# Performance work log

Hardware: AMD Instinct MI355X
Metric: run time of the kernel (lower is better)

Reference implementation:

```python
import jax, jax.numpy as jnp
import numpy as np

N, D, NH, NC, B, NL = 400, 256, 4, 2, 64, 2
HD = D // NH


def _ln(x, g, b, eps=1e-5):
    mu = x.mean(-1, keepdims=True)
    var = ((x - mu) ** 2).mean(-1, keepdims=True)
    return (x - mu) * jax.lax.rsqrt(var + eps) * g + b


def _mha(q, kv, wqkv, bqkv, wo, bo):
    # torch nn.MultiheadAttention (batch_first), eval mode
    wq, wk, wv = jnp.split(wqkv, 3, axis=0)
    bq, bk, bv = jnp.split(bqkv, 3, axis=0)
    Bsz, Sq, _ = q.shape
    Sk = kv.shape[1]
    qh = (q @ wq.T + bq).reshape(Bsz, Sq, NH, HD).transpose(0, 2, 1, 3)
    kh = (kv @ wk.T + bk).reshape(Bsz, Sk, NH, HD).transpose(0, 2, 1, 3)
    vh = (kv @ wv.T + bv).reshape(Bsz, Sk, NH, HD).transpose(0, 2, 1, 3)
    scores = jnp.einsum('bhqd,bhkd->bhqk', qh, kh) / jnp.sqrt(jnp.float32(HD))
    attn = jax.nn.softmax(scores, axis=-1)
    o = jnp.einsum('bhqk,bhkd->bhqd', attn, vh)
    o = o.transpose(0, 2, 1, 3).reshape(Bsz, Sq, D)
    return o @ wo.T + bo


def setup_inputs() -> dict:
    key = jax.random.key(0)
    ks = iter(jax.random.split(key, 64))
    w = lambda *s: (jax.random.normal(next(ks), s, dtype=jnp.float32) * 0.02)
    inp = {
        'fc_matrix': jax.random.uniform(next(ks), (B, N, N), dtype=jnp.float32),
        'sc_matrix': jax.random.uniform(next(ks), (B, N, N), dtype=jnp.float32),
        'proj_w': w(D, N), 'proj_b': jnp.zeros((D,), jnp.float32),
        'enc_qkv_w': w(NL, 3 * D, D), 'enc_qkv_b': jnp.zeros((NL, 3 * D), jnp.float32),
        'enc_out_w': w(NL, D, D), 'enc_out_b': jnp.zeros((NL, D), jnp.float32),
        'enc_lin1_w': w(NL, 4 * D, D), 'enc_lin1_b': jnp.zeros((NL, 4 * D), jnp.float32),
        'enc_lin2_w': w(NL, D, 4 * D), 'enc_lin2_b': jnp.zeros((NL, D), jnp.float32),
        'enc_n1_g': jnp.ones((NL, D), jnp.float32), 'enc_n1_b': jnp.zeros((NL, D), jnp.float32),
        'enc_n2_g': jnp.ones((NL, D), jnp.float32), 'enc_n2_b': jnp.zeros((NL, D), jnp.float32),
        'gcn_w1': w(D, N), 'gcn_b1': jnp.zeros((D,), jnp.float32),
        'gcn_w2': w(D, D), 'gcn_b2': jnp.zeros((D,), jnp.float32),
        'ca1_qkv_w': w(3 * D, D), 'ca1_qkv_b': jnp.zeros((3 * D,), jnp.float32),
        'ca1_out_w': w(D, D), 'ca1_out_b': jnp.zeros((D,), jnp.float32),
        'ca1_n_g': jnp.ones((D,), jnp.float32), 'ca1_n_b': jnp.zeros((D,), jnp.float32),
        'ca2_qkv_w': w(3 * D, D), 'ca2_qkv_b': jnp.zeros((3 * D,), jnp.float32),
        'ca2_out_w': w(D, D), 'ca2_out_b': jnp.zeros((D,), jnp.float32),
        'ca2_n_g': jnp.ones((D,), jnp.float32), 'ca2_n_b': jnp.zeros((D,), jnp.float32),
        'cls_w1': w(128, N * D), 'cls_b1': jnp.zeros((128,), jnp.float32),
        'cls_w2': w(NC, 128), 'cls_b2': jnp.zeros((NC,), jnp.float32),
    }
    return inp


def reference(fc_matrix, sc_matrix, proj_w, proj_b,
              enc_qkv_w, enc_qkv_b, enc_out_w, enc_out_b,
              enc_lin1_w, enc_lin1_b, enc_lin2_w, enc_lin2_b,
              enc_n1_g, enc_n1_b, enc_n2_g, enc_n2_b,
              gcn_w1, gcn_b1, gcn_w2, gcn_b2,
              ca1_qkv_w, ca1_qkv_b, ca1_out_w, ca1_out_b, ca1_n_g, ca1_n_b,
              ca2_qkv_w, ca2_qkv_b, ca2_out_w, ca2_out_b, ca2_n_g, ca2_n_b,
              cls_w1, cls_b1, cls_w2, cls_b2):
    # ---- FC branch: input proj + 2 post-norm transformer encoder layers ----
    h = fc_matrix @ proj_w.T + proj_b  # [B,N,D]
    for l in range(NL):
        a = _mha(h, h, enc_qkv_w[l], enc_qkv_b[l], enc_out_w[l], enc_out_b[l])
        h = _ln(h + a, enc_n1_g[l], enc_n1_b[l])
        ff = jax.nn.relu(h @ enc_lin1_w[l].T + enc_lin1_b[l]) @ enc_lin2_w[l].T + enc_lin2_b[l]
        h = _ln(h + ff, enc_n2_g[l], enc_n2_b[l])
    Z_F = h

    # ---- SC branch: dense-equivalent of per-sample nonzero()+GCNConv ----
    # all entries of sc are nonzero -> edge set == dense adjacency (self-loops present,
    # so add_remaining_self_loops is a no-op). deg = in-degree (column sums of weights).
    deg = sc_matrix.sum(axis=-2)  # [B,N]
    dinv = jnp.where(deg > 0, jax.lax.rsqrt(deg), 0.0)
    An = dinv[:, :, None] * sc_matrix * dinv[:, None, :]  # An[b,i,j] = dinv_i * w_ij * dinv_j
    h1 = jnp.einsum('bij,bid->bjd', An, sc_matrix @ gcn_w1.T) + gcn_b1  # aggregate src->dst
    h1 = jax.nn.relu(h1)
    Z_S = jnp.einsum('bij,bid->bjd', An, h1 @ gcn_w2.T) + gcn_b2  # [B,N,D]

    # ---- Cross attention (eval: dropout = identity) ----
    Z_F_cross = _ln(Z_F + _mha(Z_F, Z_S, ca1_qkv_w, ca1_qkv_b, ca1_out_w, ca1_out_b), ca1_n_g, ca1_n_b)
    Z_S_cross = _ln(Z_S + _mha(Z_S, Z_F, ca2_qkv_w, ca2_qkv_b, ca2_out_w, ca2_out_b), ca2_n_g, ca2_n_b)

    Z_joint = (Z_F_cross + Z_S_cross) * 0.5
    flat = Z_joint.reshape(Z_joint.shape[0], -1)  # [B, N*D]
    logits = jax.nn.relu(flat @ cls_w1.T + cls_b1) @ cls_w2.T + cls_b2
    return logits
```

## Files before the change

kernel.cpp:

```cpp
#include <hip/hip_runtime.h>
#include <math.h>

#define NB   64
#define NN   400
#define DD   256
#define NHH  4
#define HDD  64
#define MR   25600

typedef __attribute__((ext_vector_type(8))) short bf16x8;
typedef __attribute__((ext_vector_type(4))) float f32x4;

__device__ __forceinline__ short f2bf(float x) {
    union { float f; unsigned u; } v; v.f = x;
    return (short)((v.u + 0x7FFFu + ((v.u >> 16) & 1u)) >> 16);
}
__device__ __forceinline__ float bf2f(short s) {
    union { unsigned u; float f; } v; v.u = ((unsigned)(unsigned short)s) << 16;
    return v.f;
}
__device__ __forceinline__ void gl_lds16(const void* g, void* l) {
    __builtin_amdgcn_global_load_lds(
        (const __attribute__((address_space(1))) unsigned*)g,
        (__attribute__((address_space(3))) unsigned*)l, 16, 0, 0);
}
__device__ __forceinline__ void wait_vmcnt(int n) {
    switch (n) {
    case 0: asm volatile("s_waitcnt vmcnt(0)" ::: "memory"); break;
    case 1: asm volatile("s_waitcnt vmcnt(1)" ::: "memory"); break;
    case 2: asm volatile("s_waitcnt vmcnt(2)" ::: "memory"); break;
    case 3: asm volatile("s_waitcnt vmcnt(3)" ::: "memory"); break;
    case 4: asm volatile("s_waitcnt vmcnt(4)" ::: "memory"); break;
    default: asm volatile("s_waitcnt vmcnt(5)" ::: "memory"); break;
    }
}
__device__ __forceinline__ void barrier_raw() {
    __builtin_amdgcn_sched_barrier(0);
    __builtin_amdgcn_s_barrier();
    __builtin_amdgcn_sched_barrier(0);
}


__global__ __launch_bounds__(256) void gemm_p8(
    const short* __restrict__ A, int arows, long long sA,
    const short* __restrict__ B, int brows, long long sB,
    const float* __restrict__ bias,
    short* __restrict__ C, int crows, int crz, long long sCe,
    int M, int N, int Npad, int K, int relu)
{
    __shared__ short lds[24576];
    const int tid = threadIdx.x;
    const int z = blockIdx.z;
    const int m0 = blockIdx.x * 128, n0 = blockIdx.y * 128;
    const short* Ab = A + (size_t)z * sA;
    const short* Bb = B + (size_t)z * sB;

    const int w = tid >> 6, lane = tid & 63;
    const int quad = lane >> 4, l15 = lane & 15;
    const int wm = w & 1, wn = w >> 1;

    f32x4 acc[4][4] = {};

    const int KT = K >> 5;

    auto STAGE = [&](int buf, int kt) {
        const int gp0 = kt << 2;
        short* Al = lds + buf * 8192;
        short* Bl = Al + 4096;
#pragma unroll
        for (int i = 0; i < 4; ++i) {
            int c = i * 4 + w;
            int p = (c >> 1) & 3, hh = c & 1;
            if (c < 8)
                gl_lds16(Ab + ((size_t)(gp0 + p) * arows + m0 + hh * 64 + lane) * 8,
                         &Al[(p * 128 + hh * 64) * 8]);
            else
                gl_lds16(Bb + ((size_t)(gp0 + p) * brows + n0 + hh * 64 + lane) * 8,
                         &Bl[(p * 128 + hh * 64) * 8]);
        }
    };

    STAGE(0, 0);
    STAGE(1, 1);
    for (int kt = 0; kt < KT; ++kt) {
        wait_vmcnt(kt + 1 < KT ? 4 : 0);
        barrier_raw();
        if (kt + 2 < KT) STAGE((kt + 2) % 3, kt + 2);
        const short* Al = lds + (kt % 3) * 8192;
        const short* Bl = Al + 4096;
        bf16x8 af[4], bfr[4];
#pragma unroll
        for (int mi = 0; mi < 4; ++mi)
            af[mi] = *reinterpret_cast<const bf16x8*>(
                &Al[(quad * 128 + wm * 64 + mi * 16 + l15) * 8]);
#pragma unroll
        for (int ni = 0; ni < 4; ++ni)
            bfr[ni] = *reinterpret_cast<const bf16x8*>(
                &Bl[(quad * 128 + wn * 64 + ni * 16 + l15) * 8]);
#pragma unroll
        for (int mi = 0; mi < 4; ++mi)
#pragma unroll
            for (int ni = 0; ni < 4; ++ni)
                acc[mi][ni] = __builtin_amdgcn_mfma_f32_16x16x32_bf16(af[mi], bfr[ni], acc[mi][ni], 0, 0, 0);
    }
    __syncthreads();

#pragma unroll
    for (int mi = 0; mi < 4; ++mi) {
#pragma unroll
        for (int r = 0; r < 4; ++r) {
            int row = wm * 64 + mi * 16 + quad * 4 + r;
#pragma unroll
            for (int ni = 0; ni < 4; ++ni) {
                int col = wn * 64 + ni * 16 + l15;
                int gcol = n0 + col;
                float v = 0.0f;
                if (gcol < N) {
                    v = acc[mi][ni][r];
                    if (bias) v += bias[gcol];
                    if (relu) v = fmaxf(v, 0.0f);
                }
                lds[row * 136 + col] = f2bf(v);
            }
        }
    }
    __syncthreads();
    short* Cbz = C + (size_t)z * sCe;
    const long long zr = (long long)z * crz;
#pragma unroll
    for (int t = 0; t < 8; ++t) {
        int c = t * 256 + tid;
        int row = c & 127, p16 = c >> 7;
        int grow = m0 + row;
        int gcol0 = n0 + p16 * 8;
        if (grow < M && gcol0 < Npad) {
            bf16x8 v = *reinterpret_cast<const bf16x8*>(&lds[row * 136 + p16 * 8]);
            *reinterpret_cast<bf16x8*>(
                &Cbz[((size_t)(gcol0 >> 3) * crows + zr + grow) * 8]) = v;
        }
    }
}

__global__ __launch_bounds__(256) void gemm_ln(
    const short* __restrict__ A,
    const short* __restrict__ B, int brows,
    const float* __restrict__ bias,
    const short* __restrict__ resid,
    const float* __restrict__ g, const float* __restrict__ bb,
    short* __restrict__ out, int K)
{
    __shared__ short lds[30720];
    __shared__ float gs[256], bs[256], bi_s[256];
    __shared__ float red[2][4][64];
    const int tid = threadIdx.x;
    const int m0 = blockIdx.x * 64;
    const int w = tid >> 6, lane = tid & 63;
    const int quad = lane >> 4, l15 = lane & 15;
    gs[tid] = g[tid]; bs[tid] = bb[tid]; bi_s[tid] = bias[tid];

    f32x4 acc[16] = {};
    const int KT = K >> 5;

    auto STAGE = [&](int buf, int kt) {
        const int gp0 = kt << 2;
        short* Al = lds + buf * 10240;
        short* Bl = Al + 2048;
#pragma unroll
        for (int i = 0; i < 5; ++i) {
            int c = i * 4 + w;
            if (c < 4) {
                gl_lds16(A + ((size_t)(gp0 + c) * MR + m0 + lane) * 8, &Al[(c * 64) * 8]);
            } else {
                int cb = c - 4, p = cb >> 2, cq = cb & 3;
                gl_lds16(B + ((size_t)(gp0 + p) * brows + cq * 64 + lane) * 8,
                         &Bl[(p * 256 + cq * 64) * 8]);
            }
        }
    };

    STAGE(0, 0);
    STAGE(1, 1);
    for (int kt = 0; kt < KT; ++kt) {
        wait_vmcnt(kt + 1 < KT ? 5 : 0);
        barrier_raw();
        if (kt + 2 < KT) STAGE((kt + 2) % 3, kt + 2);
        const short* Al = lds + (kt % 3) * 10240;
        const short* Bl = Al + 2048;
        bf16x8 af = *reinterpret_cast<const bf16x8*>(
            &Al[(quad * 64 + w * 16 + l15) * 8]);
#pragma unroll
        for (int ni = 0; ni < 16; ++ni) {
            bf16x8 bfr = *reinterpret_cast<const bf16x8*>(
                &Bl[(quad * 256 + ni * 16 + l15) * 8]);
            acc[ni] = __builtin_amdgcn_mfma_f32_16x16x32_bf16(af, bfr, acc[ni], 0, 0, 0);
        }
    }
    __syncthreads();

    short* rowt = lds;
#pragma unroll
    for (int ni = 0; ni < 16; ++ni) {
        int col = ni * 16 + l15;
        int part = col >> 6, idx = col & 63;
#pragma unroll
        for (int r = 0; r < 4; ++r) {
            int row = w * 16 + quad * 4 + r;
            rowt[row * 264 + part * 66 + idx] = f2bf(acc[ni][r] + bi_s[col]);
        }
    }
    __syncthreads();

    const int row = tid >> 2, part = tid & 3;
    const int grow = m0 + row;
    float vv[8][8];
    float sum = 0.0f, sq = 0.0f;
#pragma unroll
    for (int i = 0; i < 8; ++i) {
        int plane = part * 8 + i;
        bf16x8 rv = *reinterpret_cast<const bf16x8*>(resid + ((size_t)plane * MR + grow) * 8);
        bf16x8 tv = *reinterpret_cast<const bf16x8*>(&rowt[row * 264 + part * 66 + i * 8]);
#pragma unroll
        for (int e = 0; e < 8; ++e) {
            float v = bf2f(tv[e]) + bf2f(rv[e]);
            vv[i][e] = v; sum += v; sq += v * v;
        }
    }
    red[0][part][row] = sum; red[1][part][row] = sq;
    __syncthreads();
    sum = red[0][0][row] + red[0][1][row] + red[0][2][row] + red[0][3][row];
    sq  = red[1][0][row] + red[1][1][row] + red[1][2][row] + red[1][3][row];
    float mu = sum * (1.0f / 256.0f);
    float var = sq * (1.0f / 256.0f) - mu * mu;
    float rstd = 1.0f / sqrtf(fmaxf(var, 0.0f) + 1e-5f);
#pragma unroll
    for (int i = 0; i < 8; ++i) {
        int plane = part * 8 + i;
        bf16x8 o;
#pragma unroll
        for (int e = 0; e < 8; ++e)
            o[e] = f2bf((vv[i][e] - mu) * rstd * gs[plane * 8 + e] + bs[plane * 8 + e]);
        *reinterpret_cast<bf16x8*>(out + ((size_t)plane * MR + grow) * 8) = o;
    }
}

__global__ __launch_bounds__(256) void vtrans(
    const short* __restrict__ qkv, short* __restrict__ vT)
{
    __shared__ short tile[64][66];
    const int id = blockIdx.x;
    const int xcd = id & 7, rem = id >> 3;
    const int bh_hi = rem / 7, c = rem - bh_hi * 7;
    const int bh_i = bh_hi * 8 + xcd;
    const int h = bh_i & 3, b = bh_i >> 2;
    const int tid = threadIdx.x;
    const size_t bh = (size_t)bh_i;
    for (int t = tid; t < 512; t += 256) {
        int pp = t >> 6, l = t & 63;
        int j = c * 64 + l;
        bf16x8 v;
        if (j < NN)
            v = *reinterpret_cast<const bf16x8*>(
                qkv + (((size_t)(64 + 8 * h + pp)) * MR + (size_t)b * NN + j) * 8);
        else { for (int e = 0; e < 8; ++e) v[e] = 0; }
#pragma unroll
        for (int e = 0; e < 8; ++e) tile[l][pp * 8 + e] = v[e];
    }
    __syncthreads();
    for (int t = tid; t < 512; t += 256) {
        int kq = t >> 6, d = t & 63;
        int kp = c * 8 + kq;
        bf16x8 o;
#pragma unroll
        for (int e = 0; e < 8; ++e) o[e] = tile[kq * 8 + e][d];
        *reinterpret_cast<bf16x8*>(vT + ((bh * 56 + kp) * 64 + d) * 8) = o;
    }
}

__global__ __launch_bounds__(256) void attn_p8(
    const short* __restrict__ qkv, const short* __restrict__ vT,
    short* __restrict__ Out)
{
    __shared__ short KP[8 * 448 * 8];
    __shared__ short QV[5][2048];
    const int id = blockIdx.x;
    const int xcd = id & 7, rem = id >> 3;
    const int bh_hi = rem / 7, qt = rem - bh_hi * 7;
    const int bh_i = bh_hi * 8 + xcd;
    const int h = bh_i & 3, b = bh_i >> 2;
    const int tid = threadIdx.x;
    const int w = tid >> 6, lane = tid & 63;
    const int quad = lane >> 4, l15 = lane & 15;
    const size_t rowb = (size_t)b * NN;

    short* Qs = &QV[0][0];
    for (int j = w; j < 8; j += 4)
        gl_lds16(qkv + (((size_t)(8 * h + j)) * MR + rowb + qt * 64 + lane) * 8, &Qs[j * 512]);
    for (int t = w; t < 56; t += 4) {
        int j = t / 7, c = t - j * 7;
        gl_lds16(qkv + (((size_t)(32 + 8 * h + j)) * MR + rowb + c * 64 + lane) * 8,
                 &KP[(j * 448 + c * 64) * 8]);
    }
    __syncthreads();

    bf16x8 aq0 = *reinterpret_cast<const bf16x8*>(&Qs[(quad * 64 + w * 16 + l15) * 8]);
    bf16x8 aq1 = *reinterpret_cast<const bf16x8*>(&Qs[((4 + quad) * 64 + w * 16 + l15) * 8]);
    __syncthreads();
#pragma unroll
    for (int c = 0; c < 4; ++c)
        gl_lds16(vT + (((size_t)bh_i * 56 + c * 4 + w) * 64 + lane) * 8, &QV[c][w * 512]);

    f32x4 sacc[25];
#pragma unroll
    for (int nt = 0; nt < 25; ++nt) { sacc[nt][0] = 0; sacc[nt][1] = 0; sacc[nt][2] = 0; sacc[nt][3] = 0; }
#pragma unroll
    for (int nt = 0; nt < 25; ++nt) {
        bf16x8 b0 = *reinterpret_cast<const bf16x8*>(&KP[(quad * 448 + nt * 16 + l15) * 8]);
        bf16x8 b1 = *reinterpret_cast<const bf16x8*>(&KP[((4 + quad) * 448 + nt * 16 + l15) * 8]);
        sacc[nt] = __builtin_amdgcn_mfma_f32_16x16x32_bf16(aq0, b0, sacc[nt], 0, 0, 0);
        sacc[nt] = __builtin_amdgcn_mfma_f32_16x16x32_bf16(aq1, b1, sacc[nt], 0, 0, 0);
    }

    float mx[4] = {-3e38f, -3e38f, -3e38f, -3e38f}, sm[4] = {0, 0, 0, 0};
#pragma unroll
    for (int nt = 0; nt < 25; ++nt)
#pragma unroll
        for (int r = 0; r < 4; ++r) mx[r] = fmaxf(mx[r], sacc[nt][r]);
#pragma unroll
    for (int r = 0; r < 4; ++r) {
        mx[r] = fmaxf(mx[r], __shfl_xor(mx[r], 1));
        mx[r] = fmaxf(mx[r], __shfl_xor(mx[r], 2));
        mx[r] = fmaxf(mx[r], __shfl_xor(mx[r], 4));
        mx[r] = fmaxf(mx[r], __shfl_xor(mx[r], 8));
    }
#pragma unroll
    for (int nt = 0; nt < 25; ++nt)
#pragma unroll
        for (int r = 0; r < 4; ++r) {
            float e = __expf((sacc[nt][r] - mx[r]) * 0.125f);
            sacc[nt][r] = e;
            sm[r] += e;
        }
#pragma unroll
    for (int r = 0; r < 4; ++r) {
        sm[r] += __shfl_xor(sm[r], 1);
        sm[r] += __shfl_xor(sm[r], 2);
        sm[r] += __shfl_xor(sm[r], 4);
        sm[r] += __shfl_xor(sm[r], 8);
    }
    __syncthreads();

#pragma unroll
    for (int nt = 0; nt < 25; ++nt)
#pragma unroll
        for (int r = 0; r < 4; ++r) {
            int colk = nt * 16 + l15;
            KP[((colk >> 3) * 64 + w * 16 + quad * 4 + r) * 8 + (colk & 7)] = f2bf(sacc[nt][r]);
        }
    for (int idx = tid; idx < 1024; idx += 256) KP[25600 + idx] = 0;

    f32x4 oacc[4];
#pragma unroll
    for (int dt = 0; dt < 4; ++dt) { oacc[dt][0] = 0; oacc[dt][1] = 0; oacc[dt][2] = 0; oacc[dt][3] = 0; }
    __syncthreads();

#pragma unroll
    for (int c = 0; c < 13; ++c) {
        wait_vmcnt((12 - c) < 3 ? (12 - c) : 3);
        barrier_raw();
        if (c + 4 <= 12)
            gl_lds16(vT + (((size_t)bh_i * 56 + (c + 4) * 4 + w) * 64 + lane) * 8,
                     &QV[(c + 4) % 5][w * 512]);
        bf16x8 pa = *reinterpret_cast<const bf16x8*>(
            &KP[((c * 4 + quad) * 64 + w * 16 + l15) * 8]);
#pragma unroll
        for (int dt = 0; dt < 4; ++dt) {
            bf16x8 vb = *reinterpret_cast<const bf16x8*>(
                &QV[c % 5][quad * 512 + (dt * 16 + l15) * 8]);
            oacc[dt] = __builtin_amdgcn_mfma_f32_16x16x32_bf16(pa, vb, oacc[dt], 0, 0, 0);
        }
    }
#pragma unroll
    for (int r = 0; r < 4; ++r) {
        int row = qt * 64 + w * 16 + quad * 4 + r;
        if (row >= NN) continue;
        float inv = 1.0f / sm[r];
#pragma unroll
        for (int dt = 0; dt < 4; ++dt) {
            int col = dt * 16 + l15;
            Out[(((size_t)(8 * h + (col >> 3))) * MR + rowb + row) * 8 + (col & 7)] =
                f2bf(oacc[dt][r] * inv);
        }
    }
}

__global__ void conv_p8(const float* __restrict__ src, short* __restrict__ dst,
                        int R, int K, int Kp, int PR)
{
    const int G = Kp >> 3;
    int idx = blockIdx.x * 256 + threadIdx.x;
    if (idx >= R * G) return;
    int r = idx / G, g = idx - r * G;
    int k0 = g << 3;
    bf16x8 o;
    if (k0 + 8 <= K) {
        const float4 v0 = *reinterpret_cast<const float4*>(src + (size_t)r * K + k0);
        const float4 v1 = *reinterpret_cast<const float4*>(src + (size_t)r * K + k0 + 4);
        o[0] = f2bf(v0.x); o[1] = f2bf(v0.y); o[2] = f2bf(v0.z); o[3] = f2bf(v0.w);
        o[4] = f2bf(v1.x); o[5] = f2bf(v1.y); o[6] = f2bf(v1.z); o[7] = f2bf(v1.w);
    } else {
#pragma unroll
        for (int e = 0; e < 8; ++e) {
            int k = k0 + e;
            o[e] = (k < K) ? f2bf(src[(size_t)r * K + k]) : (short)0;
        }
    }
    *reinterpret_cast<bf16x8*>(dst + ((size_t)g * PR + r) * 8) = o;
}

__global__ __launch_bounds__(256) void w1_p8(
    const float* __restrict__ W1, short* __restrict__ Wp)
{
    __shared__ float tile[128][129];
    const int k0 = blockIdx.x * 128;
    const int tid = threadIdx.x;
    for (int t = 0; t < 16; ++t) {
        int idx = t * 256 + tid;
        int r = idx >> 5, k4 = idx & 31;
        float4 v = *(const float4*)(W1 + (size_t)r * 102400 + k0 + k4 * 4);
        tile[r][k4 * 4 + 0] = v.x; tile[r][k4 * 4 + 1] = v.y;
        tile[r][k4 * 4 + 2] = v.z; tile[r][k4 * 4 + 3] = v.w;
    }
    __syncthreads();
    for (int t = 0; t < 8; ++t) {
        int idx = t * 256 + tid;
        int pidx = idx >> 7, r = idx & 127;
        bf16x8 o;
#pragma unroll
        for (int e = 0; e < 8; ++e) o[e] = f2bf(tile[r][pidx * 8 + e]);
        *reinterpret_cast<bf16x8*>(Wp + (((size_t)(k0 >> 3) + pidx) * 128 + r) * 8) = o;
    }
}

__global__ void colsum_dinv(const float* __restrict__ sc, float* __restrict__ dinv)
{
    int b = blockIdx.y;
    int j = blockIdx.x * 256 + threadIdx.x;
    if (j >= NN) return;
    const float* p = sc + (size_t)b * NN * NN + j;
    float s = 0.0f;
    for (int i = 0; i < NN; ++i) s += p[(size_t)i * NN];
    dinv[b * NN + j] = (s > 0.0f) ? 1.0f / sqrtf(s) : 0.0f;
}

__global__ __launch_bounds__(256) void sc_prep(
    const float* __restrict__ sc, const float* __restrict__ dinv,
    short* __restrict__ scb, short* __restrict__ anT)
{
    __shared__ float tile[64][65];
    const int b = blockIdx.z;
    const int i0 = blockIdx.y * 64, j0 = blockIdx.x * 64;
    const int tid = threadIdx.x;
    const float* sb = sc + (size_t)b * NN * NN;
    short* scbb = scb + (size_t)b * 56 * 512 * 8;
    short* anTb = anT + (size_t)b * 56 * 512 * 8;
    for (int e = tid; e < 4096; e += 256) {
        int r = e >> 6, c = e & 63;
        int i = i0 + r, j = j0 + c;
        tile[r][c] = (i < NN && j < NN) ? sb[(size_t)i * NN + j] : 0.0f;
    }
    __syncthreads();
    for (int e = tid; e < 4096; e += 256) {
        int r = e >> 6, c = e & 63;
        int i = i0 + r, j = j0 + c;
        scbb[((size_t)(j >> 3) * 512 + i) * 8 + (j & 7)] = f2bf(tile[r][c]);
        float v = 0.0f;
        if (i < NN && j < NN) v = tile[r][c] * dinv[b * NN + i] * dinv[b * NN + j];
        anTb[((size_t)(i >> 3) * 512 + j) * 8 + (i & 7)] = f2bf(v);
    }
}

__global__ __launch_bounds__(256) void cls_gemm(
    const short* __restrict__ C1, const short* __restrict__ C2,
    const short* __restrict__ Wp, float* __restrict__ partial)
{
    __shared__ short Al[32 * 64 * 8];
    __shared__ short Wl[8 * 128 * 8];
    const int j = blockIdx.x;
    const int tid = threadIdx.x;
    const int w = tid >> 6, lane = tid & 63;
    const int quad = lane >> 4, l15 = lane & 15;

    for (int s = 0; s < 8; ++s) {
        int idx = s * 256 + tid;
        int p = idx >> 6, b = idx & 63;
        size_t ad = ((size_t)p * MR + (size_t)b * NN + j) * 8;
        bf16x8 a = *reinterpret_cast<const bf16x8*>(C1 + ad);
        bf16x8 c = *reinterpret_cast<const bf16x8*>(C2 + ad);
        bf16x8 o;
#pragma unroll
        for (int e = 0; e < 8; ++e) o[e] = f2bf(0.5f * (bf2f(a[e]) + bf2f(c[e])));
        *reinterpret_cast<bf16x8*>(&Al[(p * 64 + b) * 8]) = o;
    }

    f32x4 acc[4][2] = {};
    const size_t wp0 = (size_t)j * 32;
    for (int s = 0; s < 4; ++s) {
#pragma unroll
        for (int pp = 0; pp < 2; ++pp) {
            int p = w + pp * 4;
            gl_lds16(Wp + ((wp0 + s * 8 + p) * 128 + lane) * 8,      &Wl[(p * 128) * 8]);
            gl_lds16(Wp + ((wp0 + s * 8 + p) * 128 + 64 + lane) * 8, &Wl[(p * 128 + 64) * 8]);
        }
        __syncthreads();
#pragma unroll
        for (int kb = 0; kb < 2; ++kb) {
            bf16x8 af[4], bfr[2];
#pragma unroll
            for (int mi = 0; mi < 4; ++mi)
                af[mi] = *reinterpret_cast<const bf16x8*>(
                    &Al[((s * 8 + kb * 4 + quad) * 64 + mi * 16 + l15) * 8]);
#pragma unroll
            for (int ni = 0; ni < 2; ++ni)
                bfr[ni] = *reinterpret_cast<const bf16x8*>(
                    &Wl[((kb * 4 + quad) * 128 + w * 32 + ni * 16 + l15) * 8]);
#pragma unroll
            for (int mi = 0; mi < 4; ++mi)
#pragma unroll
                for (int ni = 0; ni < 2; ++ni)
                    acc[mi][ni] = __builtin_amdgcn_mfma_f32_16x16x32_bf16(af[mi], bfr[ni], acc[mi][ni], 0, 0, 0);
        }
        __syncthreads();
    }
    float* pj = partial + (size_t)j * 8192;
#pragma unroll
    for (int mi = 0; mi < 4; ++mi)
#pragma unroll
        for (int r = 0; r < 4; ++r) {
            int row = mi * 16 + quad * 4 + r;
#pragma unroll
            for (int ni = 0; ni < 2; ++ni)
                pj[row * 128 + w * 32 + ni * 16 + l15] = acc[mi][ni][r];
        }
}

__global__ void cls_reduce(const float* __restrict__ partial, float* __restrict__ clsh)
{
    int o = blockIdx.x * 256 + threadIdx.x;
    float s = 0.0f;
    for (int kb = 0; kb < 400; ++kb) s += partial[(size_t)kb * 8192 + o];
    clsh[o] = s;
}

__global__ void logits_final(
    const float* __restrict__ clsh, const float* __restrict__ b1,
    const float* __restrict__ w2, const float* __restrict__ b2,
    float* __restrict__ out)
{
    __shared__ float t[128];
    int b = blockIdx.x;
    int tid = threadIdx.x;
    t[tid] = fmaxf(clsh[b * 128 + tid] + b1[tid], 0.0f);
    __syncthreads();
    if (tid < 2) {
        float s = b2[tid];
        for (int o = 0; o < 128; ++o) s += t[o] * w2[tid * 128 + o];
        out[b * 2 + tid] = s;
    }
}

extern "C" void kernel_launch(void* const* d_in, const int* in_sizes, int n_in,
                              void* d_out, int out_size, void* d_ws, size_t ws_size,
                              hipStream_t stream)
{
    const float* fc        = (const float*)d_in[0];
    const float* sc        = (const float*)d_in[1];
    const float* proj_w    = (const float*)d_in[2];
    const float* proj_b    = (const float*)d_in[3];
    const float* enc_qkv_w = (const float*)d_in[4];
    const float* enc_qkv_b = (const float*)d_in[5];
    const float* enc_out_w = (const float*)d_in[6];
    const float* enc_out_b = (const float*)d_in[7];
    const float* enc_l1_w  = (const float*)d_in[8];
    const float* enc_l1_b  = (const float*)d_in[9];
    const float* enc_l2_w  = (const float*)d_in[10];
    const float* enc_l2_b  = (const float*)d_in[11];
    const float* enc_n1_g  = (const float*)d_in[12];
    const float* enc_n1_b  = (const float*)d_in[13];
    const float* enc_n2_g  = (const float*)d_in[14];
    const float* enc_n2_b  = (const float*)d_in[15];
    const float* gcn_w1    = (const float*)d_in[16];
    const float* gcn_b1    = (const float*)d_in[17];
    const float* gcn_w2    = (const float*)d_in[18];
    const float* gcn_b2    = (const float*)d_in[19];
    const float* ca1_qkv_w = (const float*)d_in[20];
    const float* ca1_qkv_b = (const float*)d_in[21];
    const float* ca1_out_w = (const float*)d_in[22];
    const float* ca1_out_b = (const float*)d_in[23];
    const float* ca1_n_g   = (const float*)d_in[24];
    const float* ca1_n_b   = (const float*)d_in[25];
    const float* ca2_qkv_w = (const float*)d_in[26];
    const float* ca2_qkv_b = (const float*)d_in[27];
    const float* ca2_out_w = (const float*)d_in[28];
    const float* ca2_out_b = (const float*)d_in[29];
    const float* ca2_n_g   = (const float*)d_in[30];
    const float* ca2_n_b   = (const float*)d_in[31];
    const float* cls_w1    = (const float*)d_in[32];
    const float* cls_b1    = (const float*)d_in[33];
    const float* cls_w2    = (const float*)d_in[34];
    const float* cls_b2    = (const float*)d_in[35];

    char* wsb = (char*)d_ws;
    size_t off = 0;
    auto alloc = [&](size_t bytes) { char* r = wsb + off; off += (bytes + 255) & ~(size_t)255; return r; };
    short* bufBig = (short*)alloc((size_t)MR * 1024 * 2);
    short* fcb    = (short*)alloc((size_t)56 * MR * 8 * 2);
    short* anT    = (short*)alloc((size_t)NB * 56 * 512 * 8 * 2);
    short* bufH   = (short*)alloc((size_t)32 * MR * 8 * 2);
    short* bufA   = (short*)alloc((size_t)32 * MR * 8 * 2);
    short* bufC   = (short*)alloc((size_t)32 * MR * 8 * 2);
    short* bufZS  = (short*)alloc((size_t)32 * MR * 8 * 2);
    short* vT     = (short*)alloc((size_t)NB * NHH * 56 * 64 * 8 * 2);
    short* w1b    = (short*)alloc((size_t)12800 * 128 * 8 * 2);
    short* projwb = (short*)alloc((size_t)56 * 256 * 8 * 2);
    short* qkvwb  = (short*)alloc((size_t)32 * 1536 * 8 * 2);
    short* outwb  = (short*)alloc((size_t)32 * 512 * 8 * 2);
    short* l1wb   = (short*)alloc((size_t)32 * 2048 * 8 * 2);
    short* l2wb   = (short*)alloc((size_t)128 * 512 * 8 * 2);
    short* gw1b   = (short*)alloc((size_t)56 * 256 * 8 * 2);
    short* gw2b   = (short*)alloc((size_t)32 * 256 * 8 * 2);
    short* c1qb   = (short*)alloc((size_t)32 * 768 * 8 * 2);
    short* c1ob   = (short*)alloc((size_t)32 * 256 * 8 * 2);
    short* c2qb   = (short*)alloc((size_t)32 * 768 * 8 * 2);
    short* c2ob   = (short*)alloc((size_t)32 * 256 * 8 * 2);
    float* dinv   = (float*)alloc((size_t)MR * 4);
    float* clsh   = (float*)alloc((size_t)NB * 128 * 4);
    short* scb = bufBig;
    short* XT1 = bufBig + (size_t)64 * 56 * 512 * 8;
    short* h1  = bufBig;
    short* XT2 = XT1;
    float* partial = (float*)fcb;

    dim3 blk(256);
    auto cgrid = [](long long n) { return dim3((unsigned)((n + 255) / 256)); };

    conv_p8<<<cgrid((long long)MR * 56), blk, 0, stream>>>(fc, fcb, MR, 400, 448, MR);
    conv_p8<<<cgrid(256 * 56), blk, 0, stream>>>(proj_w, projwb, 256, 400, 448, 256);
    conv_p8<<<cgrid(1536 * 32), blk, 0, stream>>>(enc_qkv_w, qkvwb, 1536, 256, 256, 1536);
    conv_p8<<<cgrid(512 * 32), blk, 0, stream>>>(enc_out_w, outwb, 512, 256, 256, 512);
    conv_p8<<<cgrid(2048 * 32), blk, 0, stream>>>(enc_l1_w, l1wb, 2048, 256, 256, 2048);
    conv_p8<<<cgrid(512 * 128), blk, 0, stream>>>(enc_l2_w, l2wb, 512, 1024, 1024, 512);
    conv_p8<<<cgrid(256 * 56), blk, 0, stream>>>(gcn_w1, gw1b, 256, 400, 448, 256);
    conv_p8<<<cgrid(256 * 32), blk, 0, stream>>>(gcn_w2, gw2b, 256, 256, 256, 256);
    conv_p8<<<cgrid(768 * 32), blk, 0, stream>>>(ca1_qkv_w, c1qb, 768, 256, 256, 768);
    conv_p8<<<cgrid(256 * 32), blk, 0, stream>>>(ca1_out_w, c1ob, 256, 256, 256, 256);
    conv_p8<<<cgrid(768 * 32), blk, 0, stream>>>(ca2_qkv_w, c2qb, 768, 256, 256, 768);
    conv_p8<<<cgrid(256 * 32), blk, 0, stream>>>(ca2_out_w, c2ob, 256, 256, 256, 256);
    w1_p8<<<800, blk, 0, stream>>>(cls_w1, w1b);

    gemm_p8<<<dim3(200, 2, 1), blk, 0, stream>>>(
        fcb, MR, 0, projwb, 256, 0, proj_b, bufH, MR, 0, 0, MR, 256, 256, 448, 0);
    for (int l = 0; l < 2; ++l) {
        gemm_p8<<<dim3(200, 6, 1), blk, 0, stream>>>(
            bufH, MR, 0, qkvwb + (size_t)l * 768 * 8, 1536, 0, enc_qkv_b + l * 768,
            bufBig, MR, 0, 0, MR, 768, 768, 256, 0);
        vtrans<<<dim3(1792), blk, 0, stream>>>(bufBig, vT);
        attn_p8<<<dim3(1792), blk, 0, stream>>>(bufBig, vT, bufA);
        gemm_ln<<<400, blk, 0, stream>>>(
            bufA, outwb + (size_t)l * 256 * 8, 512, enc_out_b + l * 256,
            bufH, enc_n1_g + l * DD, enc_n1_b + l * DD, bufH, 256);
        gemm_p8<<<dim3(200, 8, 1), blk, 0, stream>>>(
            bufH, MR, 0, l1wb + (size_t)l * 1024 * 8, 2048, 0, enc_l1_b + l * 1024,
            bufBig, MR, 0, 0, MR, 1024, 1024, 256, 1);
        gemm_ln<<<400, blk, 0, stream>>>(
            bufBig, l2wb + (size_t)l * 256 * 8, 512, enc_l2_b + l * 256,
            bufH, enc_n2_g + l * DD, enc_n2_b + l * DD, bufH, 1024);
    }

    colsum_dinv<<<dim3(2, NB), blk, 0, stream>>>(sc, dinv);
    sc_prep<<<dim3(7, 7, NB), blk, 0, stream>>>(sc, dinv, scb, anT);
    gemm_p8<<<dim3(2, 4, NB), blk, 0, stream>>>(
        gw1b, 256, 0, scb, 512, 56LL * 512 * 8, nullptr,
        XT1, 256, 0, 56LL * 256 * 8, 256, 400, 448, 448, 0);
    gemm_p8<<<dim3(4, 2, NB), blk, 0, stream>>>(
        anT, 512, 56LL * 512 * 8, XT1, 256, 56LL * 256 * 8, gcn_b1,
        h1, 512, 0, 32LL * 512 * 8, 400, 256, 256, 448, 1);
    gemm_p8<<<dim3(2, 4, NB), blk, 0, stream>>>(
        gw2b, 256, 0, h1, 512, 32LL * 512 * 8, nullptr,
        XT2, 256, 0, 56LL * 256 * 8, 256, 400, 448, 256, 0);
    gemm_p8<<<dim3(4, 2, NB), blk, 0, stream>>>(
        anT, 512, 56LL * 512 * 8, XT2, 256, 56LL * 256 * 8, gcn_b2,
        bufZS, MR, 400, 0, 400, 256, 256, 448, 0);

    gemm_p8<<<dim3(200, 2, 1), blk, 0, stream>>>(
        bufH, MR, 0, c1qb, 768, 0, ca1_qkv_b, bufBig, MR, 0, 0, MR, 256, 256, 256, 0);
    gemm_p8<<<dim3(200, 4, 1), blk, 0, stream>>>(
        bufZS, MR, 0, c1qb + 256 * 8, 768, 0, ca1_qkv_b + 256,
        bufBig + (size_t)32 * MR * 8, MR, 0, 0, MR, 512, 512, 256, 0);
    vtrans<<<dim3(1792), blk, 0, stream>>>(bufBig, vT);
    attn_p8<<<dim3(1792), blk, 0, stream>>>(bufBig, vT, bufA);
    gemm_ln<<<400, blk, 0, stream>>>(
        bufA, c1ob, 256, ca1_out_b, bufH, ca1_n_g, ca1_n_b, bufC, 256);

    gemm_p8<<<dim3(200, 2, 1), blk, 0, stream>>>(
        bufZS, MR, 0, c2qb, 768, 0, ca2_qkv_b, bufBig, MR, 0, 0, MR, 256, 256, 256, 0);
    gemm_p8<<<dim3(200, 4, 1), blk, 0, stream>>>(
        bufH, MR, 0, c2qb + 256 * 8, 768, 0, ca2_qkv_b + 256,
        bufBig + (size_t)32 * MR * 8, MR, 0, 0, MR, 512, 512, 256, 0);
    vtrans<<<dim3(1792), blk, 0, stream>>>(bufBig, vT);
    attn_p8<<<dim3(1792), blk, 0, stream>>>(bufBig, vT, bufA);
    gemm_ln<<<400, blk, 0, stream>>>(
        bufA, c2ob, 256, ca2_out_b, bufZS, ca2_n_g, ca2_n_b, bufZS, 256);

    cls_gemm<<<400, blk, 0, stream>>>(bufC, bufZS, w1b, partial);
    cls_reduce<<<32, blk, 0, stream>>>(partial, clsh);
    logits_final<<<NB, 128, 0, stream>>>(clsh, cls_b1, cls_w2, cls_b2, (float*)d_out);
}
```

Baseline: 1.020 ms.

## Read K and V directly from global memory in attention kernel, shrink LDS

The attention kernel no longer stages K and the pipelined V chunks through LDS. Each lane now loads its MFMA B-operands straight from global memory (likely L2-resident), and only the probability tile stays in a single smaller shared buffer. Launch bounds now request 3 blocks per CU, aiming for higher occupancy and fewer barriers. The risk is more global/L2 traffic and exposed load latency, since the explicit vmcnt-based V pipelining is gone.

```diff
diff --git a/kernel.cpp b/kernel.cpp
--- a/kernel.cpp
+++ b/kernel.cpp
@@ -276,12 +276,11 @@
     }
 }
 
-__global__ __launch_bounds__(256) void attn_p8(
+__global__ __launch_bounds__(256, 3) void attn_p8(
     const short* __restrict__ qkv, const short* __restrict__ vT,
     short* __restrict__ Out)
 {
-    __shared__ short KP[8 * 448 * 8];
-    __shared__ short QV[5][2048];
+    __shared__ short PS[26624];
     const int id = blockIdx.x;
     const int xcd = id & 7, rem = id >> 3;
     const int bh_hi = rem / 7, qt = rem - bh_hi * 7;
@@ -292,30 +291,23 @@
     const int quad = lane >> 4, l15 = lane & 15;
     const size_t rowb = (size_t)b * NN;
 
-    short* Qs = &QV[0][0];
     for (int j = w; j < 8; j += 4)
-        gl_lds16(qkv + (((size_t)(8 * h + j)) * MR + rowb + qt * 64 + lane) * 8, &Qs[j * 512]);
-    for (int t = w; t < 56; t += 4) {
-        int j = t / 7, c = t - j * 7;
-        gl_lds16(qkv + (((size_t)(32 + 8 * h + j)) * MR + rowb + c * 64 + lane) * 8,
-                 &KP[(j * 448 + c * 64) * 8]);
-    }
-    __syncthreads();
-
-    bf16x8 aq0 = *reinterpret_cast<const bf16x8*>(&Qs[(quad * 64 + w * 16 + l15) * 8]);
-    bf16x8 aq1 = *reinterpret_cast<const bf16x8*>(&Qs[((4 + quad) * 64 + w * 16 + l15) * 8]);
-    __syncthreads();
-#pragma unroll
-    for (int c = 0; c < 4; ++c)
-        gl_lds16(vT + (((size_t)bh_i * 56 + c * 4 + w) * 64 + lane) * 8, &QV[c][w * 512]);
+        gl_lds16(qkv + (((size_t)(8 * h + j)) * MR + rowb + qt * 64 + lane) * 8, &PS[j * 512]);
+    __syncthreads();
+
+    bf16x8 aq0 = *reinterpret_cast<const bf16x8*>(&PS[(quad * 64 + w * 16 + l15) * 8]);
+    bf16x8 aq1 = *reinterpret_cast<const bf16x8*>(&PS[((4 + quad) * 64 + w * 16 + l15) * 8]);
+
+    const short* Kb0 = qkv + ((size_t)(32 + 8 * h + quad) * MR + rowb + l15) * 8;
+    const short* Kb1 = qkv + ((size_t)(36 + 8 * h + quad) * MR + rowb + l15) * 8;
 
     f32x4 sacc[25];
 #pragma unroll
     for (int nt = 0; nt < 25; ++nt) { sacc[nt][0] = 0; sacc[nt][1] = 0; sacc[nt][2] = 0; sacc[nt][3] = 0; }
 #pragma unroll
     for (int nt = 0; nt < 25; ++nt) {
-        bf16x8 b0 = *reinterpret_cast<const bf16x8*>(&KP[(quad * 448 + nt * 16 + l15) * 8]);
-        bf16x8 b1 = *reinterpret_cast<const bf16x8*>(&KP[((4 + quad) * 448 + nt * 16 + l15) * 8]);
+        bf16x8 b0 = *reinterpret_cast<const bf16x8*>(Kb0 + nt * 128);
+        bf16x8 b1 = *reinterpret_cast<const bf16x8*>(Kb1 + nt * 128);
         sacc[nt] = __builtin_amdgcn_mfma_f32_16x16x32_bf16(aq0, b0, sacc[nt], 0, 0, 0);
         sacc[nt] = __builtin_amdgcn_mfma_f32_16x16x32_bf16(aq1, b1, sacc[nt], 0, 0, 0);
     }
@@ -354,28 +346,23 @@
 #pragma unroll
         for (int r = 0; r < 4; ++r) {
             int colk = nt * 16 + l15;
-            KP[((colk >> 3) * 64 + w * 16 + quad * 4 + r) * 8 + (colk & 7)] = f2bf(sacc[nt][r]);
-        }
-    for (int idx = tid; idx < 1024; idx += 256) KP[25600 + idx] = 0;
+            PS[((colk >> 3) * 64 + w * 16 + quad * 4 + r) * 8 + (colk & 7)] = f2bf(sacc[nt][r]);
+        }
+    for (int idx = tid; idx < 1024; idx += 256) PS[25600 + idx] = 0;
 
     f32x4 oacc[4];
 #pragma unroll
     for (int dt = 0; dt < 4; ++dt) { oacc[dt][0] = 0; oacc[dt][1] = 0; oacc[dt][2] = 0; oacc[dt][3] = 0; }
     __syncthreads();
 
-#pragma unroll
-    for (int c = 0; c < 13; ++c) {
-        wait_vmcnt((12 - c) < 3 ? (12 - c) : 3);
-        barrier_raw();
-        if (c + 4 <= 12)
-            gl_lds16(vT + (((size_t)bh_i * 56 + (c + 4) * 4 + w) * 64 + lane) * 8,
-                     &QV[(c + 4) % 5][w * 512]);
+    const short* Vb = vT + (((size_t)bh_i * 56 + quad) * 64 + l15) * 8;
+#pragma unroll
+    for (int kt = 0; kt < 13; ++kt) {
         bf16x8 pa = *reinterpret_cast<const bf16x8*>(
-            &KP[((c * 4 + quad) * 64 + w * 16 + l15) * 8]);
+            &PS[((kt * 4 + quad) * 64 + w * 16 + l15) * 8]);
 #pragma unroll
         for (int dt = 0; dt < 4; ++dt) {
-            bf16x8 vb = *reinterpret_cast<const bf16x8*>(
-                &QV[c % 5][quad * 512 + (dt * 16 + l15) * 8]);
+            bf16x8 vb = *reinterpret_cast<const bf16x8*>(Vb + kt * 2048 + dt * 128);
             oacc[dt] = __builtin_amdgcn_mfma_f32_16x16x32_bf16(pa, vb, oacc[dt], 0, 0, 0);
         }
     }
```

New measurement: 974.2 us. 4.5% less time.
